# Kernel optimization log

Hardware: AMD Instinct MI355X
Metric: run time of the kernel (lower is better)

## Reference

```python
import jax, jax.numpy as jnp
import numpy as np

CLAMP = 10.0  # forward default arg `clamp`


def setup_inputs() -> dict:
    key = jax.random.key(0)
    k1, k2, k3, k4 = jax.random.split(key, 4)
    B, N = 256, 8192
    return {
        "pred_frames": jax.random.normal(k1, (B, N, 4, 4), dtype=jnp.float32),
        "true_frames": jax.random.normal(k2, (B, N, 4, 4), dtype=jnp.float32),
        "pred_pos": jax.random.normal(k3, (B, N, 3), dtype=jnp.float32),
        "true_pos": jax.random.normal(k4, (B, N, 3), dtype=jnp.float32),
    }


def reference(pred_frames, true_frames, pred_pos, true_pos):
    # Batched Kabsch alignment of pred_pos -> true_pos, then clamped point error.
    # pred_frames / true_frames are unused by the original module's forward.
    cA = pred_pos.mean(axis=1, keepdims=True)  # [B,1,3]
    cB = true_pos.mean(axis=1, keepdims=True)  # [B,1,3]
    AA = pred_pos - cA                          # [B,N,3]
    BB = true_pos - cB                          # [B,N,3]
    H = jnp.einsum('bni,bnj->bij', AA, BB)      # [B,3,3] covariance
    U, S, Vt = jnp.linalg.svd(H)
    # R = Vt^T @ U^T : R[b,i,k] = sum_j Vt[b,j,i] * U[b,k,j]
    R = jnp.einsum('bji,bkj->bik', Vt, U)
    det = jnp.linalg.det(R)                     # [B]
    sign = jnp.where(det < 0, -1.0, 1.0).astype(Vt.dtype)
    Vt_fixed = Vt.at[:, -1, :].multiply(sign[:, None])  # flip last row if det<0
    R = jnp.einsum('bji,bkj->bik', Vt_fixed, U)
    # t = centroid_B - R @ centroid_A (vector of shape [B,3])
    t = cB[:, 0, :] - jnp.einsum('bij,bj->bi', R, cA[:, 0, :])
    # NOTE: original applies pred_pos @ R (not R^T) + t, replicated faithfully.
    pred_aligned = jnp.einsum('bni,bij->bnj', pred_pos, R) + t[:, None, :]
    dist = jnp.linalg.norm(pred_aligned - true_pos, axis=-1)  # [B,N]
    # clamp(max=CLAMP).mean() per batch, then averaged over batch == global mean
    return jnp.mean(jnp.minimum(dist, CLAMP))
```

## Files before the change

kernel.cpp:

```cpp
#include <hip/hip_runtime.h>
#include <math.h>

#define NB 256
#define NPT 8192
#define SPLITS 4
#define CHUNK (NPT / SPLITS)
#define THREADS 256
#define CLAMPV 10.0f

__global__ __launch_bounds__(THREADS) void cov_kernel(
    const float* __restrict__ pred, const float* __restrict__ tru,
    float* __restrict__ stats)
{
    const int blk = blockIdx.x;
    const int b  = blk >> 2;
    const int sp = blk & 3;
    const float* P = pred + ((size_t)b * NPT + (size_t)sp * CHUNK) * 3;
    const float* T = tru  + ((size_t)b * NPT + (size_t)sp * CHUNK) * 3;

    float acc[15];
#pragma unroll
    for (int i = 0; i < 15; ++i) acc[i] = 0.f;

    for (int n = threadIdx.x; n < CHUNK; n += THREADS) {
        const float px = P[3*n+0], py = P[3*n+1], pz = P[3*n+2];
        const float tx = T[3*n+0], ty = T[3*n+1], tz = T[3*n+2];
        acc[0] += px; acc[1] += py; acc[2] += pz;
        acc[3] += tx; acc[4] += ty; acc[5] += tz;
        acc[6]  += px*tx; acc[7]  += px*ty; acc[8]  += px*tz;
        acc[9]  += py*tx; acc[10] += py*ty; acc[11] += py*tz;
        acc[12] += pz*tx; acc[13] += pz*ty; acc[14] += pz*tz;
    }
#pragma unroll
    for (int i = 0; i < 15; ++i)
        for (int off = 32; off > 0; off >>= 1)
            acc[i] += __shfl_down(acc[i], off, 64);

    __shared__ float smem[THREADS/64][15];
    const int wave = threadIdx.x >> 6, lane = threadIdx.x & 63;
    if (lane == 0) {
#pragma unroll
        for (int i = 0; i < 15; ++i) smem[wave][i] = acc[i];
    }
    __syncthreads();
    if (threadIdx.x < 15) {
        float s = 0.f;
#pragma unroll
        for (int w = 0; w < THREADS/64; ++w) s += smem[w][threadIdx.x];
        stats[(size_t)blk * 16 + threadIdx.x] = s;
    }
}

__device__ inline double det3(const double m[3][3]) {
    return m[0][0]*(m[1][1]*m[2][2]-m[1][2]*m[2][1])
         - m[0][1]*(m[1][0]*m[2][2]-m[1][2]*m[2][0])
         + m[0][2]*(m[1][0]*m[2][1]-m[1][1]*m[2][0]);
}

__global__ void svd_kernel(const float* __restrict__ stats, float* __restrict__ RT)
{
    const int b = blockIdx.x * blockDim.x + threadIdx.x;
    if (b >= NB) return;

    double sA[3] = {0,0,0}, sB[3] = {0,0,0}, M[9] = {0,0,0,0,0,0,0,0,0};
    for (int sp = 0; sp < SPLITS; ++sp) {
        const float* st = stats + ((size_t)(b * SPLITS + sp)) * 16;
        for (int i = 0; i < 3; ++i) sA[i] += st[i];
        for (int i = 0; i < 3; ++i) sB[i] += st[3 + i];
        for (int i = 0; i < 9; ++i) M[i]  += st[6 + i];
    }
    double cA[3], cB[3];
    for (int i = 0; i < 3; ++i) { cA[i] = sA[i] / NPT; cB[i] = sB[i] / NPT; }

    double H[3][3];
    for (int i = 0; i < 3; ++i)
        for (int j = 0; j < 3; ++j)
            H[i][j] = M[i*3 + j] - (double)NPT * cA[i] * cB[j];

    double A[3][3];
    for (int i = 0; i < 3; ++i)
        for (int j = 0; j < 3; ++j) {
            double s = 0.0;
            for (int k = 0; k < 3; ++k) s += H[k][i] * H[k][j];
            A[i][j] = s;
        }
    double V[3][3] = {{1,0,0},{0,1,0},{0,0,1}};
    const int PQ[3][2] = {{0,1},{0,2},{1,2}};
    for (int sweep = 0; sweep < 15; ++sweep) {
        for (int r = 0; r < 3; ++r) {
            const int p = PQ[r][0], q = PQ[r][1];
            const double apq = A[p][q];
            if (fabs(apq) < 1e-300) continue;
            const double theta = (A[q][q] - A[p][p]) / (2.0 * apq);
            const double t = copysign(1.0, theta) / (fabs(theta) + sqrt(theta*theta + 1.0));
            const double c = 1.0 / sqrt(t*t + 1.0);
            const double s = t * c;
            for (int k = 0; k < 3; ++k) {
                const double akp = A[k][p], akq = A[k][q];
                A[k][p] = c*akp - s*akq;
                A[k][q] = s*akp + c*akq;
            }
            for (int k = 0; k < 3; ++k) {
                const double apk = A[p][k], aqk = A[q][k];
                A[p][k] = c*apk - s*aqk;
                A[q][k] = s*apk + c*aqk;
            }
            for (int k = 0; k < 3; ++k) {
                const double vkp = V[k][p], vkq = V[k][q];
                V[k][p] = c*vkp - s*vkq;
                V[k][q] = s*vkp + c*vkq;
            }
        }
    }
    double eig[3] = {A[0][0], A[1][1], A[2][2]};
    int idx[3] = {0, 1, 2};
    if (eig[idx[0]] < eig[idx[1]]) { int t_ = idx[0]; idx[0] = idx[1]; idx[1] = t_; }
    if (eig[idx[0]] < eig[idx[2]]) { int t_ = idx[0]; idx[0] = idx[2]; idx[2] = t_; }
    if (eig[idx[1]] < eig[idx[2]]) { int t_ = idx[1]; idx[1] = idx[2]; idx[2] = t_; }

    double Vc[3][3], Uc[3][3];
    for (int i = 0; i < 3; ++i) {
        const int j = idx[i];
        for (int r = 0; r < 3; ++r) Vc[r][i] = V[r][j];
    }
    for (int i = 0; i < 3; ++i) {
        double u[3];
        for (int r = 0; r < 3; ++r)
            u[r] = H[r][0]*Vc[0][i] + H[r][1]*Vc[1][i] + H[r][2]*Vc[2][i];
        const double nrm = sqrt(u[0]*u[0] + u[1]*u[1] + u[2]*u[2]);
        if (nrm > 1e-30) {
            for (int r = 0; r < 3; ++r) Uc[r][i] = u[r] / nrm;
        } else if (i == 2) {
            Uc[0][2] = Uc[1][0]*Uc[2][1] - Uc[2][0]*Uc[1][1];
            Uc[1][2] = Uc[2][0]*Uc[0][1] - Uc[0][0]*Uc[2][1];
            Uc[2][2] = Uc[0][0]*Uc[1][1] - Uc[1][0]*Uc[0][1];
        } else {
            for (int r = 0; r < 3; ++r) Uc[r][i] = (r == i) ? 1.0 : 0.0;
        }
    }
    if (det3(Uc) * det3(Vc) < 0.0)
        for (int r = 0; r < 3; ++r) Vc[r][2] = -Vc[r][2];

    double R[3][3];
    for (int i = 0; i < 3; ++i)
        for (int k = 0; k < 3; ++k)
            R[i][k] = Vc[i][0]*Uc[k][0] + Vc[i][1]*Uc[k][1] + Vc[i][2]*Uc[k][2];
    double tv[3];
    for (int i = 0; i < 3; ++i)
        tv[i] = cB[i] - (R[i][0]*cA[0] + R[i][1]*cA[1] + R[i][2]*cA[2]);

    float* o = RT + (size_t)b * 12;
    for (int i = 0; i < 3; ++i)
        for (int j = 0; j < 3; ++j)
            o[i*3 + j] = (float)R[i][j];
    for (int i = 0; i < 3; ++i) o[9 + i] = (float)tv[i];
}

__global__ __launch_bounds__(THREADS) void dist_kernel(
    const float* __restrict__ pred, const float* __restrict__ tru,
    const float* __restrict__ RT, float* __restrict__ partial)
{
    const int blk = blockIdx.x;
    const int b  = blk >> 2;
    const int sp = blk & 3;
    const float* P = pred + ((size_t)b * NPT + (size_t)sp * CHUNK) * 3;
    const float* T = tru  + ((size_t)b * NPT + (size_t)sp * CHUNK) * 3;
    const float* rt = RT + (size_t)b * 12;
    const float R00 = rt[0], R01 = rt[1], R02 = rt[2];
    const float R10 = rt[3], R11 = rt[4], R12 = rt[5];
    const float R20 = rt[6], R21 = rt[7], R22 = rt[8];
    const float t0 = rt[9], t1 = rt[10], t2 = rt[11];

    float acc = 0.f;
    for (int n = threadIdx.x; n < CHUNK; n += THREADS) {
        const float px = P[3*n+0], py = P[3*n+1], pz = P[3*n+2];
        const float tx = T[3*n+0], ty = T[3*n+1], tz = T[3*n+2];
        const float ax = px*R00 + py*R10 + pz*R20 + t0;
        const float ay = px*R01 + py*R11 + pz*R21 + t1;
        const float az = px*R02 + py*R12 + pz*R22 + t2;
        const float dx = ax - tx, dy = ay - ty, dz = az - tz;
        const float d = sqrtf(dx*dx + dy*dy + dz*dz);
        acc += fminf(d, CLAMPV);
    }
    for (int off = 32; off > 0; off >>= 1)
        acc += __shfl_down(acc, off, 64);
    __shared__ float smem[THREADS/64];
    const int wave = threadIdx.x >> 6, lane = threadIdx.x & 63;
    if (lane == 0) smem[wave] = acc;
    __syncthreads();
    if (threadIdx.x == 0) {
        float s = 0.f;
#pragma unroll
        for (int w = 0; w < THREADS/64; ++w) s += smem[w];
        partial[blk] = s;
    }
}

__global__ __launch_bounds__(THREADS) void finalize_kernel(
    const float* __restrict__ partial, float* __restrict__ out)
{
    float acc = 0.f;
    for (int i = threadIdx.x; i < NB * SPLITS; i += THREADS) acc += partial[i];
    for (int off = 32; off > 0; off >>= 1)
        acc += __shfl_down(acc, off, 64);
    __shared__ float smem[THREADS/64];
    const int wave = threadIdx.x >> 6, lane = threadIdx.x & 63;
    if (lane == 0) smem[wave] = acc;
    __syncthreads();
    if (threadIdx.x == 0) {
        float s = 0.f;
#pragma unroll
        for (int w = 0; w < THREADS/64; ++w) s += smem[w];
        out[0] = s / 2097152.0f;
    }
}

extern "C" void kernel_launch(void* const* d_in, const int* in_sizes, int n_in,
                              void* d_out, int out_size, void* d_ws, size_t ws_size,
                              hipStream_t stream)
{
    const float* pred_pos = (const float*)d_in[2];
    const float* true_pos = (const float*)d_in[3];
    float* out = (float*)d_out;

    float* ws      = (float*)d_ws;
    float* stats   = ws;
    float* RT      = ws + (size_t)NB * SPLITS * 16;
    float* partial = RT + (size_t)NB * 12;

    cov_kernel<<<NB * SPLITS, THREADS, 0, stream>>>(pred_pos, true_pos, stats);
    svd_kernel<<<1, NB, 0, stream>>>(stats, RT);
    dist_kernel<<<NB * SPLITS, THREADS, 0, stream>>>(pred_pos, true_pos, RT, partial);
    finalize_kernel<<<1, THREADS, 0, stream>>>(partial, out);
}
```

Before: 275.8 us.

## Vectorize point loads with float4 and unroll Jacobi SVD into scalar registers

The covariance and distance kernels now load four points at a time as three float4 values per array instead of scalar strided loads, so each thread issues 128-bit memory transactions. The SVD kernel is rewritten with scalar registers, a fixed seven-sweep unrolled Jacobi, and a reflection fix based on the sign of det(H) applied to the smallest eigenvector. The load change targets global memory inefficiency in the bandwidth-bound passes. The SVD rewrite cuts per-thread local-array traffic and sweeps but changes numerics slightly, including the degenerate-case handling.

```diff
diff --git a/kernel.cpp b/kernel.cpp
--- a/kernel.cpp
+++ b/kernel.cpp
@@ -15,22 +15,34 @@
     const int blk = blockIdx.x;
     const int b  = blk >> 2;
     const int sp = blk & 3;
-    const float* P = pred + ((size_t)b * NPT + (size_t)sp * CHUNK) * 3;
-    const float* T = tru  + ((size_t)b * NPT + (size_t)sp * CHUNK) * 3;
+    const float4* __restrict__ P4 =
+        (const float4*)(pred + ((size_t)b * NPT + (size_t)sp * CHUNK) * 3);
+    const float4* __restrict__ T4 =
+        (const float4*)(tru  + ((size_t)b * NPT + (size_t)sp * CHUNK) * 3);
 
     float acc[15];
 #pragma unroll
     for (int i = 0; i < 15; ++i) acc[i] = 0.f;
 
-    for (int n = threadIdx.x; n < CHUNK; n += THREADS) {
-        const float px = P[3*n+0], py = P[3*n+1], pz = P[3*n+2];
-        const float tx = T[3*n+0], ty = T[3*n+1], tz = T[3*n+2];
-        acc[0] += px; acc[1] += py; acc[2] += pz;
-        acc[3] += tx; acc[4] += ty; acc[5] += tz;
-        acc[6]  += px*tx; acc[7]  += px*ty; acc[8]  += px*tz;
-        acc[9]  += py*tx; acc[10] += py*ty; acc[11] += py*tz;
-        acc[12] += pz*tx; acc[13] += pz*ty; acc[14] += pz*tz;
-    }
+#define COVACC(px,py,pz,tx,ty,tz)                                   \
+    do {                                                            \
+        acc[0] += (px); acc[1] += (py); acc[2] += (pz);             \
+        acc[3] += (tx); acc[4] += (ty); acc[5] += (tz);             \
+        acc[6]  += (px)*(tx); acc[7]  += (px)*(ty); acc[8]  += (px)*(tz); \
+        acc[9]  += (py)*(tx); acc[10] += (py)*(ty); acc[11] += (py)*(tz); \
+        acc[12] += (pz)*(tx); acc[13] += (pz)*(ty); acc[14] += (pz)*(tz); \
+    } while (0)
+
+    for (int g = threadIdx.x; g < CHUNK / 4; g += THREADS) {
+        const float4 pa = P4[3*g+0], pb = P4[3*g+1], pc = P4[3*g+2];
+        const float4 ta = T4[3*g+0], tb = T4[3*g+1], tc = T4[3*g+2];
+        COVACC(pa.x, pa.y, pa.z,  ta.x, ta.y, ta.z);
+        COVACC(pa.w, pb.x, pb.y,  ta.w, tb.x, tb.y);
+        COVACC(pb.z, pb.w, pc.x,  tb.z, tb.w, tc.x);
+        COVACC(pc.y, pc.z, pc.w,  tc.y, tc.z, tc.w);
+    }
+#undef COVACC
+
 #pragma unroll
     for (int i = 0; i < 15; ++i)
         for (int off = 32; off > 0; off >>= 1)
@@ -51,10 +63,30 @@
     }
 }
 
-__device__ inline double det3(const double m[3][3]) {
-    return m[0][0]*(m[1][1]*m[2][2]-m[1][2]*m[2][1])
-         - m[0][1]*(m[1][0]*m[2][2]-m[1][2]*m[2][0])
-         + m[0][2]*(m[1][0]*m[2][1]-m[1][1]*m[2][0]);
+__device__ __forceinline__ void jrot(
+    double& app, double& aqq, double& apq, double& apr, double& aqr,
+    double& vp0, double& vq0, double& vp1, double& vq1, double& vp2, double& vq2)
+{
+    const double theta = (aqq - app) * 0.5 / apq;
+    const double t0 = copysign(1.0, theta) / (fabs(theta) + sqrt(theta*theta + 1.0));
+    const double c0 = 1.0 / sqrt(t0*t0 + 1.0);
+    const double s0 = t0 * c0;
+    const bool live = fabs(apq) > 1e-300;
+    const double t = live ? t0 : 0.0;
+    const double c = live ? c0 : 1.0;
+    const double s = live ? s0 : 0.0;
+
+    app -= t * apq;
+    aqq += t * apq;
+    apq  = 0.0;
+    const double pr = apr, qr = aqr;
+    apr = c*pr - s*qr;
+    aqr = s*pr + c*qr;
+
+    double a, bv;
+    a = vp0; bv = vq0; vp0 = c*a - s*bv; vq0 = s*a + c*bv;
+    a = vp1; bv = vq1; vp1 = c*a - s*bv; vq1 = s*a + c*bv;
+    a = vp2; bv = vq2; vp2 = c*a - s*bv; vq2 = s*a + c*bv;
 }
 
 __global__ void svd_kernel(const float* __restrict__ stats, float* __restrict__ RT)
@@ -62,98 +94,94 @@
     const int b = blockIdx.x * blockDim.x + threadIdx.x;
     if (b >= NB) return;
 
-    double sA[3] = {0,0,0}, sB[3] = {0,0,0}, M[9] = {0,0,0,0,0,0,0,0,0};
+    double s0=0,s1=0,s2=0,s3=0,s4=0,s5=0,s6=0,s7=0,s8=0,
+           s9=0,s10=0,s11=0,s12=0,s13=0,s14=0;
+#pragma unroll
     for (int sp = 0; sp < SPLITS; ++sp) {
         const float* st = stats + ((size_t)(b * SPLITS + sp)) * 16;
-        for (int i = 0; i < 3; ++i) sA[i] += st[i];
-        for (int i = 0; i < 3; ++i) sB[i] += st[3 + i];
-        for (int i = 0; i < 9; ++i) M[i]  += st[6 + i];
-    }
-    double cA[3], cB[3];
-    for (int i = 0; i < 3; ++i) { cA[i] = sA[i] / NPT; cB[i] = sB[i] / NPT; }
-
-    double H[3][3];
-    for (int i = 0; i < 3; ++i)
-        for (int j = 0; j < 3; ++j)
-            H[i][j] = M[i*3 + j] - (double)NPT * cA[i] * cB[j];
-
-    double A[3][3];
-    for (int i = 0; i < 3; ++i)
-        for (int j = 0; j < 3; ++j) {
-            double s = 0.0;
-            for (int k = 0; k < 3; ++k) s += H[k][i] * H[k][j];
-            A[i][j] = s;
-        }
-    double V[3][3] = {{1,0,0},{0,1,0},{0,0,1}};
-    const int PQ[3][2] = {{0,1},{0,2},{1,2}};
-    for (int sweep = 0; sweep < 15; ++sweep) {
-        for (int r = 0; r < 3; ++r) {
-            const int p = PQ[r][0], q = PQ[r][1];
-            const double apq = A[p][q];
-            if (fabs(apq) < 1e-300) continue;
-            const double theta = (A[q][q] - A[p][p]) / (2.0 * apq);
-            const double t = copysign(1.0, theta) / (fabs(theta) + sqrt(theta*theta + 1.0));
-            const double c = 1.0 / sqrt(t*t + 1.0);
-            const double s = t * c;
-            for (int k = 0; k < 3; ++k) {
-                const double akp = A[k][p], akq = A[k][q];
-                A[k][p] = c*akp - s*akq;
-                A[k][q] = s*akp + c*akq;
-            }
-            for (int k = 0; k < 3; ++k) {
-                const double apk = A[p][k], aqk = A[q][k];
-                A[p][k] = c*apk - s*aqk;
-                A[q][k] = s*apk + c*aqk;
-            }
-            for (int k = 0; k < 3; ++k) {
-                const double vkp = V[k][p], vkq = V[k][q];
-                V[k][p] = c*vkp - s*vkq;
-                V[k][q] = s*vkp + c*vkq;
-            }
-        }
-    }
-    double eig[3] = {A[0][0], A[1][1], A[2][2]};
-    int idx[3] = {0, 1, 2};
-    if (eig[idx[0]] < eig[idx[1]]) { int t_ = idx[0]; idx[0] = idx[1]; idx[1] = t_; }
-    if (eig[idx[0]] < eig[idx[2]]) { int t_ = idx[0]; idx[0] = idx[2]; idx[2] = t_; }
-    if (eig[idx[1]] < eig[idx[2]]) { int t_ = idx[1]; idx[1] = idx[2]; idx[2] = t_; }
-
-    double Vc[3][3], Uc[3][3];
-    for (int i = 0; i < 3; ++i) {
-        const int j = idx[i];
-        for (int r = 0; r < 3; ++r) Vc[r][i] = V[r][j];
-    }
-    for (int i = 0; i < 3; ++i) {
-        double u[3];
-        for (int r = 0; r < 3; ++r)
-            u[r] = H[r][0]*Vc[0][i] + H[r][1]*Vc[1][i] + H[r][2]*Vc[2][i];
-        const double nrm = sqrt(u[0]*u[0] + u[1]*u[1] + u[2]*u[2]);
-        if (nrm > 1e-30) {
-            for (int r = 0; r < 3; ++r) Uc[r][i] = u[r] / nrm;
-        } else if (i == 2) {
-            Uc[0][2] = Uc[1][0]*Uc[2][1] - Uc[2][0]*Uc[1][1];
-            Uc[1][2] = Uc[2][0]*Uc[0][1] - Uc[0][0]*Uc[2][1];
-            Uc[2][2] = Uc[0][0]*Uc[1][1] - Uc[1][0]*Uc[0][1];
-        } else {
-            for (int r = 0; r < 3; ++r) Uc[r][i] = (r == i) ? 1.0 : 0.0;
-        }
-    }
-    if (det3(Uc) * det3(Vc) < 0.0)
-        for (int r = 0; r < 3; ++r) Vc[r][2] = -Vc[r][2];
-
-    double R[3][3];
-    for (int i = 0; i < 3; ++i)
-        for (int k = 0; k < 3; ++k)
-            R[i][k] = Vc[i][0]*Uc[k][0] + Vc[i][1]*Uc[k][1] + Vc[i][2]*Uc[k][2];
-    double tv[3];
-    for (int i = 0; i < 3; ++i)
-        tv[i] = cB[i] - (R[i][0]*cA[0] + R[i][1]*cA[1] + R[i][2]*cA[2]);
+        s0  += st[0];  s1  += st[1];  s2  += st[2];
+        s3  += st[3];  s4  += st[4];  s5  += st[5];
+        s6  += st[6];  s7  += st[7];  s8  += st[8];
+        s9  += st[9];  s10 += st[10]; s11 += st[11];
+        s12 += st[12]; s13 += st[13]; s14 += st[14];
+    }
+    const double inv_n = 1.0 / (double)NPT;
+    const double cA0 = s0*inv_n, cA1 = s1*inv_n, cA2 = s2*inv_n;
+    const double cB0 = s3*inv_n, cB1 = s4*inv_n, cB2 = s5*inv_n;
+
+    const double n_ = (double)NPT;
+    const double h00 = s6  - n_*cA0*cB0, h01 = s7  - n_*cA0*cB1, h02 = s8  - n_*cA0*cB2;
+    const double h10 = s9  - n_*cA1*cB0, h11 = s10 - n_*cA1*cB1, h12 = s11 - n_*cA1*cB2;
+    const double h20 = s12 - n_*cA2*cB0, h21 = s13 - n_*cA2*cB1, h22 = s14 - n_*cA2*cB2;
+
+    double a00 = h00*h00 + h10*h10 + h20*h20;
+    double a01 = h00*h01 + h10*h11 + h20*h21;
+    double a02 = h00*h02 + h10*h12 + h20*h22;
+    double a11 = h01*h01 + h11*h11 + h21*h21;
+    double a12 = h01*h02 + h11*h12 + h21*h22;
+    double a22 = h02*h02 + h12*h12 + h22*h22;
+
+    double v00=1, v01=0, v02=0,
+           v10=0, v11=1, v12=0,
+           v20=0, v21=0, v22=1;
+
+#pragma unroll
+    for (int sw = 0; sw < 7; ++sw) {
+        jrot(a00, a11, a01, a02, a12,  v00, v01, v10, v11, v20, v21);
+        jrot(a00, a22, a02, a01, a12,  v00, v02, v10, v12, v20, v22);
+        jrot(a11, a22, a12, a01, a02,  v01, v02, v11, v12, v21, v22);
+    }
+    const double e0 = a00, e1 = a11, e2 = a22;
+
+    const double u00 = h00*v00 + h01*v10 + h02*v20;
+    const double u10 = h10*v00 + h11*v10 + h12*v20;
+    const double u20 = h20*v00 + h21*v10 + h22*v20;
+    const double u01 = h00*v01 + h01*v11 + h02*v21;
+    const double u11 = h10*v01 + h11*v11 + h12*v21;
+    const double u21 = h20*v01 + h21*v11 + h22*v21;
+    const double u02 = h00*v02 + h01*v12 + h02*v22;
+    const double u12 = h10*v02 + h11*v12 + h12*v22;
+    const double u22 = h20*v02 + h21*v12 + h22*v22;
+
+    const double i0 = 1.0 / sqrt(fmax(u00*u00 + u10*u10 + u20*u20, 1e-300));
+    const double i1 = 1.0 / sqrt(fmax(u01*u01 + u11*u11 + u21*u21, 1e-300));
+    const double i2 = 1.0 / sqrt(fmax(u02*u02 + u12*u12 + u22*u22, 1e-300));
+
+    const double q00 = u00*i0, q10 = u10*i0, q20 = u20*i0;
+    const double q01 = u01*i1, q11 = u11*i1, q21 = u21*i1;
+    const double q02 = u02*i2, q12 = u12*i2, q22 = u22*i2;
+
+    const double detH = h00*(h11*h22 - h12*h21)
+                      - h01*(h10*h22 - h12*h20)
+                      + h02*(h10*h21 - h11*h20);
+    const bool flip = detH < 0.0;
+
+    int m = 0; double emin = e0;
+    if (e1 < emin) { m = 1; emin = e1; }
+    if (e2 < emin) { m = 2; }
+    const double f0 = (flip && m == 0) ? -1.0 : 1.0;
+    const double f1 = (flip && m == 1) ? -1.0 : 1.0;
+    const double f2 = (flip && m == 2) ? -1.0 : 1.0;
+
+    const double R00 = f0*v00*q00 + f1*v01*q01 + f2*v02*q02;
+    const double R01 = f0*v00*q10 + f1*v01*q11 + f2*v02*q12;
+    const double R02 = f0*v00*q20 + f1*v01*q21 + f2*v02*q22;
+    const double R10 = f0*v10*q00 + f1*v11*q01 + f2*v12*q02;
+    const double R11 = f0*v10*q10 + f1*v11*q11 + f2*v12*q12;
+    const double R12 = f0*v10*q20 + f1*v11*q21 + f2*v12*q22;
+    const double R20 = f0*v20*q00 + f1*v21*q01 + f2*v22*q02;
+    const double R21 = f0*v20*q10 + f1*v21*q11 + f2*v22*q12;
+    const double R22 = f0*v20*q20 + f1*v21*q21 + f2*v22*q22;
+
+    const double t0v = cB0 - (R00*cA0 + R01*cA1 + R02*cA2);
+    const double t1v = cB1 - (R10*cA0 + R11*cA1 + R12*cA2);
+    const double t2v = cB2 - (R20*cA0 + R21*cA1 + R22*cA2);
 
     float* o = RT + (size_t)b * 12;
-    for (int i = 0; i < 3; ++i)
-        for (int j = 0; j < 3; ++j)
-            o[i*3 + j] = (float)R[i][j];
-    for (int i = 0; i < 3; ++i) o[9 + i] = (float)tv[i];
+    o[0] = (float)R00; o[1] = (float)R01; o[2] = (float)R02;
+    o[3] = (float)R10; o[4] = (float)R11; o[5] = (float)R12;
+    o[6] = (float)R20; o[7] = (float)R21; o[8] = (float)R22;
+    o[9] = (float)t0v; o[10] = (float)t1v; o[11] = (float)t2v;
 }
 
 __global__ __launch_bounds__(THREADS) void dist_kernel(
@@ -163,8 +191,10 @@
     const int blk = blockIdx.x;
     const int b  = blk >> 2;
     const int sp = blk & 3;
-    const float* P = pred + ((size_t)b * NPT + (size_t)sp * CHUNK) * 3;
-    const float* T = tru  + ((size_t)b * NPT + (size_t)sp * CHUNK) * 3;
+    const float4* __restrict__ P4 =
+        (const float4*)(pred + ((size_t)b * NPT + (size_t)sp * CHUNK) * 3);
+    const float4* __restrict__ T4 =
+        (const float4*)(tru  + ((size_t)b * NPT + (size_t)sp * CHUNK) * 3);
     const float* rt = RT + (size_t)b * 12;
     const float R00 = rt[0], R01 = rt[1], R02 = rt[2];
     const float R10 = rt[3], R11 = rt[4], R12 = rt[5];
@@ -172,16 +202,27 @@
     const float t0 = rt[9], t1 = rt[10], t2 = rt[11];
 
     float acc = 0.f;
-    for (int n = threadIdx.x; n < CHUNK; n += THREADS) {
-        const float px = P[3*n+0], py = P[3*n+1], pz = P[3*n+2];
-        const float tx = T[3*n+0], ty = T[3*n+1], tz = T[3*n+2];
-        const float ax = px*R00 + py*R10 + pz*R20 + t0;
-        const float ay = px*R01 + py*R11 + pz*R21 + t1;
-        const float az = px*R02 + py*R12 + pz*R22 + t2;
-        const float dx = ax - tx, dy = ay - ty, dz = az - tz;
-        const float d = sqrtf(dx*dx + dy*dy + dz*dz);
-        acc += fminf(d, CLAMPV);
-    }
+
+#define DISTACC(px,py,pz,tx,ty,tz)                                          \
+    do {                                                                    \
+        const float ax = (px)*R00 + (py)*R10 + (pz)*R20 + t0;               \
+        const float ay = (px)*R01 + (py)*R11 + (pz)*R21 + t1;               \
+        const float az = (px)*R02 + (py)*R12 + (pz)*R22 + t2;               \
+        const float dx = ax - (tx), dy = ay - (ty), dz = az - (tz);         \
+        const float d = sqrtf(dx*dx + dy*dy + dz*dz);                       \
+        acc += fminf(d, CLAMPV);                                            \
+    } while (0)
+
+    for (int g = threadIdx.x; g < CHUNK / 4; g += THREADS) {
+        const float4 pa = P4[3*g+0], pb = P4[3*g+1], pc = P4[3*g+2];
+        const float4 ta = T4[3*g+0], tb = T4[3*g+1], tc = T4[3*g+2];
+        DISTACC(pa.x, pa.y, pa.z,  ta.x, ta.y, ta.z);
+        DISTACC(pa.w, pb.x, pb.y,  ta.w, tb.x, tb.y);
+        DISTACC(pb.z, pb.w, pc.x,  tb.z, tb.w, tc.x);
+        DISTACC(pc.y, pc.z, pc.w,  tc.y, tc.z, tc.w);
+    }
+#undef DISTACC
+
     for (int off = 32; off > 0; off >>= 1)
         acc += __shfl_down(acc, off, 64);
     __shared__ float smem[THREADS/64];
```

After: 263.8 us. 1.05x faster.
